# Performance work log

Hardware: AMD Instinct MI355X
Metric: run time of the kernel (lower is better)

The kernel has to match this reference:

```python
import jax, jax.numpy as jnp
import numpy as np

PS = 16          # patch size == conv kernel == stride
EPS = 1e-5       # BatchNorm eps (torch default)


def setup_inputs() -> dict:
    key = jax.random.key(0)
    ks = jax.random.split(key, 12)
    B, Cin, H = 64, 3, 256
    D, Dm = 3, 768                      # private_depth, hidden_dim
    P = (H // PS) ** 2                  # num_patches = 256

    x = jax.random.normal(ks[0], (B, Cin, H, H), jnp.float32)
    # patch-embed conv: weight [O, I, kh, kw], bias [O]
    conv0_w = jax.random.normal(ks[1], (Dm, Cin, PS, PS), jnp.float32) * 0.02
    conv0_b = jax.random.normal(ks[2], (Dm,), jnp.float32) * 0.02
    # depth x (1x1 conv + BN): stacked params
    w1 = jax.random.normal(ks[3], (D, Dm, Dm), jnp.float32) * 0.02   # [O, I]
    b1 = jax.random.normal(ks[4], (D, Dm), jnp.float32) * 0.02
    gamma = jnp.ones((D, Dm), jnp.float32)
    beta = jnp.zeros((D, Dm), jnp.float32)
    # positional embedding [1, P, Dm]
    pos_emb = jax.random.normal(ks[5], (1, P, Dm), jnp.float32)
    # mixer Linear [out, in] + bias
    mixer_w = jax.random.normal(ks[6], (Dm, Dm), jnp.float32) * 0.02
    mixer_b = jax.random.normal(ks[7], (Dm,), jnp.float32) * 0.02
    # per-sample random permutation of the P patches (replaces randperm loop)
    perm = jax.vmap(lambda k: jax.random.permutation(k, P))(
        jax.random.split(ks[8], B)).astype(jnp.int32)

    return {"x": x, "conv0_w": conv0_w, "conv0_b": conv0_b, "w1": w1,
            "b1": b1, "gamma": gamma, "beta": beta, "pos_emb": pos_emb,
            "mixer_w": mixer_w, "mixer_b": mixer_b, "perm": perm}


def reference(x, conv0_w, conv0_b, w1, b1, gamma, beta, pos_emb,
              mixer_w, mixer_b, perm):
    B, Cin, H, W = x.shape
    hp, wp = H // PS, W // PS
    Dm = conv0_w.shape[0]

    # non-overlapping patch conv == reshape + matmul
    # x -> [B, hp*wp, Cin*PS*PS] with (c, kh, kw) flattening matching conv weight
    patches = x.reshape(B, Cin, hp, PS, wp, PS).transpose(0, 2, 4, 1, 3, 5)
    patches = patches.reshape(B, hp * wp, Cin * PS * PS)
    h = jax.nn.relu(patches @ conv0_w.reshape(Dm, -1).T + conv0_b)  # [B, P, Dm]

    # private_depth x (1x1 conv -> BN (batch stats, no running stats) -> ReLU)
    for d in range(w1.shape[0]):
        h = h @ w1[d].T + b1[d]
        mu = h.mean(axis=(0, 1))                      # per-channel over (B, H*W)
        var = ((h - mu) ** 2).mean(axis=(0, 1))       # biased variance
        h = (h - mu) * jax.lax.rsqrt(var + EPS) * gamma[d] + beta[d]
        h = jax.nn.relu(h)

    # pos embedding + mixer (ReLU -> Linear)
    h = h + pos_emb
    h = jax.nn.relu(h) @ mixer_w.T + mixer_b          # [B, P, Dm]

    # per-sample pixel shuffle: shuffled[i, j] = h[i, perm[i, j]]
    out = jnp.take_along_axis(h, perm[:, :, None].astype(jnp.int32), axis=1)
    return out
```

## Files before the change

### kernel.cpp

```cpp
#include <hip/hip_runtime.h>
#include <hip/hip_bf16.h>
#include <stdint.h>

#define M_TOT 16384
#define DM 768
#define BM 128
#define BN 192
#define NKT3 12
#define QOFF (128 * DM)

typedef __attribute__((ext_vector_type(4))) float f32x4;
typedef __attribute__((ext_vector_type(8))) short short8;
typedef __attribute__((ext_vector_type(8))) unsigned short ushort8;
typedef __attribute__((ext_vector_type(4))) unsigned short ushort4v;

__device__ __forceinline__ unsigned short f2bf(float f) {
    union { float f; unsigned u; } v; v.f = f;
    unsigned r = v.u + 0x7fffu + ((v.u >> 16) & 1u);
    return (unsigned short)(r >> 16);
}
__device__ __forceinline__ float bf2f(unsigned short h) {
    union { unsigned u; float f; } v; v.u = ((unsigned)h) << 16;
    return v.f;
}

__device__ __forceinline__ void gload_lds16(const unsigned short* g, unsigned short* l) {
    __builtin_amdgcn_global_load_lds(
        (const __attribute__((address_space(1))) void*)g,
        (__attribute__((address_space(3))) void*)l, 16, 0, 0);
}

__global__ __launch_bounds__(256)
void prepw(const float* __restrict__ cw, const float* __restrict__ w1,
           const float* __restrict__ mw, const int* __restrict__ perm,
           unsigned short* __restrict__ wA, unsigned short* __restrict__ wD,
           unsigned short* __restrict__ wM, int* __restrict__ invp)
{
    int b = blockIdx.x;
    if (b < 2880) {
        int i = b * 256 + threadIdx.x;
        const float* src; unsigned short* dst; int off;
        if (i < 147456)              { src = cw; dst = wA; off = i; }
        else if (i < 147456+442368)  { src = w1; dst = wD; off = i - 147456; }
        else                         { src = mw; dst = wM; off = i - 589824; }
        f32x4 v = ((const f32x4*)src)[off];
        ushort4v o;
        o.x = f2bf(v.x); o.y = f2bf(v.y); o.z = f2bf(v.z); o.w = f2bf(v.w);
        ((ushort4v*)dst)[off] = o;
    } else {
        int i = (b - 2880) * 256 + threadIdx.x;
        int bb = i >> 8;
        invp[(bb << 8) + perm[i]] = i & 255;
    }
}

#define VM0  asm volatile("s_waitcnt vmcnt(0)" ::: "memory");
#define LGKM0 asm volatile("s_waitcnt lgkmcnt(0)" ::: "memory");
#define BARR asm volatile("s_barrier" ::: "memory");

#define PH(AB, BB, MH, KS, LOADB, PRE, POST)                                     \
  {                                                                              \
    if (LOADB) {                                                                 \
      _Pragma("unroll")                                                          \
      for (int j = 0; j < 3; ++j)                                                \
        breg[j] = *(const short8*)((const char*)Bb + (size_t)(BB) * (BN*64*2) +  \
                  (wc * 48 + j * 16 + frow) * 128 + (((KS) * 64 + fq16) ^ rswz));\
    }                                                                            \
    short8 af[4];                                                                \
    _Pragma("unroll")                                                            \
    for (int i = 0; i < 4; ++i)                                                  \
      af[i] = *(const short8*)((const char*)Aa + (size_t)(AB) * (BM*64*2) +      \
              ((MH) * 64 + i * 16 + frow) * 128 +                                \
              (((KS) * 64 + fq16) ^ rswz));                                      \
    PRE;                                                                         \
    __builtin_amdgcn_s_setprio(1);                                               \
    _Pragma("unroll")                                                            \
    for (int i = 0; i < 4; ++i)                                                  \
      _Pragma("unroll")                                                          \
      for (int j = 0; j < 3; ++j)                                                \
        acc[(MH) * 4 + i][j] = __builtin_amdgcn_mfma_f32_16x16x32_bf16(          \
            af[i], breg[j], acc[(MH) * 4 + i][j], 0, 0, 0);                      \
    __builtin_amdgcn_s_setprio(0);                                               \
    POST;                                                                        \
    BARR                                                                         \
  }

#define ALOADM(t, S)                                                             \
  {                                                                              \
    if (XF == 3) {                                                               \
      const int c  = (t) >> 2;                                                   \
      const int r  = ((t) & 3) * 64 + (lane & 7) * 8;                            \
      const int kh = r >> 4;                                                     \
      const int kw0 = r & 15;                                                    \
      _Pragma("unroll")                                                          \
      for (int j = 0; j < 4; ++j) {                                              \
        int m = m0 + rRow0 + j * 8;                                              \
        int b = m >> 8, p = m & 255;                                             \
        const float* src = X + ((((size_t)b * 3 + c) * 256 + (p >> 4) * 16 + kh) \
                                * 256 + (p & 15) * 16 + kw0);                    \
        aldf##S[j][0] = *(const f32x4*)src;                                      \
        aldf##S[j][1] = *(const f32x4*)(src + 4);                                \
      }                                                                          \
    } else {                                                                     \
      _Pragma("unroll")                                                          \
      for (int j = 0; j < 4; ++j)                                                \
        aldr##S[j] = *(const ushort8*)(gAr + (size_t)j * 8 * DM + (t) * 64);     \
    }                                                                            \
  }

#define XFORMM(t, tb, S)                                                         \
  {                                                                              \
    if (XF == 3) {                                                               \
      _Pragma("unroll")                                                          \
      for (int j = 0; j < 4; ++j) {                                              \
        int row = rRow0 + j * 8;                                                 \
        ushort8 o;                                                               \
        _Pragma("unroll")                                                        \
        for (int e = 0; e < 8; ++e)                                              \
          o[e] = f2bf((e < 4) ? aldf##S[j][0][e] : aldf##S[j][1][e - 4]);        \
        *(ushort8*)((char*)Aa + (size_t)(tb) * (BM*64*2) + row * 128 +           \
                    (((lane & 7) * 16) ^ wrswz)) = o;                            \
      }                                                                          \
    } else {                                                                     \
      const int k0 = (t) * 64 + (lane & 7) * 8;                                  \
      f32x4 sa = *(const f32x4*)(ssA + k0);                                      \
      f32x4 sb = *(const f32x4*)(ssA + k0 + 4);                                  \
      f32x4 ha = *(const f32x4*)(ssA + DM + k0);                                 \
      f32x4 hb = *(const f32x4*)(ssA + DM + k0 + 4);                             \
      _Pragma("unroll")                                                          \
      for (int j = 0; j < 4; ++j) {                                              \
        int row = rRow0 + j * 8;                                                 \
        ushort8 u = aldr##S[j];                                                  \
        ushort8 o;                                                               \
        _Pragma("unroll")                                                        \
        for (int e = 0; e < 8; ++e) {                                            \
          float f = bf2f(u[e]);                                                  \
          float sc = (e < 4) ? sa[e] : sb[e - 4];                                \
          float sh = (e < 4) ? ha[e] : hb[e - 4];                                \
          o[e] = f2bf(fmaxf(fmaf(sc, f, sh), 0.0f));                             \
        }                                                                        \
        *(ushort8*)((char*)Aa + (size_t)(tb) * (BM*64*2) + row * 128 +           \
                    (((lane & 7) * 16) ^ wrswz)) = o;                            \
      }                                                                          \
    }                                                                            \
  }

#define XTILE(kt, CB, LS, XS)                                                    \
    PH(CB, CB, 0, 0, 1, { if ((kt) < 11) STAGE_B((CB) ^ 1, (kt) + 1);            \
                          if ((kt) < 10) ALOADM((kt) + 2, LS) }, {})             \
    PH(CB, CB, 1, 0, 0, { if ((kt) < 11) XFORMM((kt) + 1, (CB) ^ 1, XS) },       \
                        { if ((kt) < 11) LGKM0 })                                \
    PH(CB, CB, 0, 1, 1, {}, {})                                                  \
    if ((kt) < 11) { PH(CB, CB, 1, 1, 0, {}, { VM0 }) }                          \
    else           { PH(CB, CB, 1, 1, 0, {}, {}) }

template<int EPI, int XF>
__global__ __launch_bounds__(256, 2)
void gemm8p(const void* __restrict__ Asrc,
            const unsigned short* __restrict__ Bw,
            const float* __restrict__ bias,
            void* __restrict__ outp,
            const int* __restrict__ invp,
            float* __restrict__ bnpart,
            const float* __restrict__ ssA)
{
    __shared__ unsigned short Aa[2][BM * 64];
    __shared__ unsigned short Bb[2][BN * 64];

    const unsigned short* A = (const unsigned short*)Asrc;
    const float* X = (const float*)Asrc;

    const int tid  = threadIdx.x;
    const int w    = tid >> 6;
    const int lane = tid & 63;
    const int wc = w;

    int bid = blockIdx.x;
    int nb  = (bid & 7) * 64 + (bid >> 3);
    const int tileM = nb >> 2, tileN = nb & 3;
    const int m0 = tileM * BM, n0 = tileN * BN;

    const int sRow = lane >> 3;
    const int swzc = ((lane & 7) * 16) ^ ((sRow & 7) << 4);
    const unsigned short* gA0 = A  + (size_t)(m0 + w * 32 + sRow) * DM + (swzc >> 1);
    const unsigned short* gB0 = Bw + (size_t)(n0 + w * 48 + sRow) * DM + (swzc >> 1);

    auto STAGE_A = [&](int buf, int kt) {
        #pragma unroll
        for (int j = 0; j < 4; ++j)
            gload_lds16(gA0 + (size_t)j * 8 * DM + kt * 64,
                        &Aa[buf][(w * 32 + j * 8) * 64]);
    };
    auto STAGE_B = [&](int buf, int kt) {
        #pragma unroll
        for (int j = 0; j < 6; ++j)
            gload_lds16(gB0 + (size_t)j * 8 * DM + kt * 64,
                        &Bb[buf][(w * 48 + j * 8) * 64]);
    };

    const int rRow0 = w * 32 + (lane >> 3);
    const unsigned short* gAr = A + (size_t)(m0 + rRow0) * DM + (lane & 7) * 8;
    const int wrswz = (lane >> 3) << 4;
    ushort8 aldr0[4], aldr1[4];
    f32x4   aldf0[4][2], aldf1[4][2];

    const int frow = lane & 15;
    const int fq16 = (lane >> 4) * 16;
    const int rswz = (lane & 7) << 4;

    f32x4 acc[8][3] = {};
    short8 breg[3];

    if (XF == 0) {
        STAGE_A(0, 0);
        STAGE_B(0, 0);
        VM0
        BARR
    } else {
        ALOADM(0, 0)
        ALOADM(1, 1)
        STAGE_B(0, 0);
        XFORMM(0, 0, 0)
        VM0
        LGKM0
        BARR
    }

    if (XF == 0) {
        #pragma unroll
        for (int kt = 0; kt < NKT3; ++kt) {
            const int cb = kt & 1, nbuf = cb ^ 1;
            PH(cb, cb, 0, 0, 1, { if (kt < 11) STAGE_B(nbuf, kt + 1); }, {})
            PH(cb, cb, 1, 0, 0, { if (kt < 11) STAGE_A(nbuf, kt + 1); }, {})
            PH(cb, cb, 0, 1, 1, {}, {})
            if (kt < 11) { PH(cb, cb, 1, 1, 0, {}, { VM0 }) }
            else         { PH(cb, cb, 1, 1, 0, {}, {}) }
        }
    } else {
        for (int kp = 0; kp < 6; ++kp) {
            const int kte = 2 * kp;
            XTILE(kte, 0, 0, 1)
            const int kto = kte + 1;
            XTILE(kto, 1, 1, 0)
        }
    }

    const int crow = (lane >> 4) * 4;
    const int ccol = lane & 15;
    const int nbase = n0 + wc * 48;

    float bv[3];
    #pragma unroll
    for (int j = 0; j < 3; ++j) bv[j] = bias[nbase + j * 16 + ccol];

    if (EPI == 0) {
        unsigned short* O = (unsigned short*)outp;
        #pragma unroll
        for (int mi = 0; mi < 8; ++mi) {
            #pragma unroll
            for (int r = 0; r < 4; ++r) {
                int m = m0 + mi * 16 + crow + r;
                unsigned short* orow = O + (size_t)m * DM + nbase + ccol;
                #pragma unroll
                for (int j = 0; j < 3; ++j)
                    orow[j * 16] = f2bf(fmaxf(acc[mi][j][r] + bv[j], 0.0f));
            }
        }
    }

    if (EPI == 2) {
        float* O = (float*)outp;
        #pragma unroll
        for (int mi = 0; mi < 8; ++mi) {
            #pragma unroll
            for (int r = 0; r < 4; ++r) {
                int m = m0 + mi * 16 + crow + r;
                int mo = (m & ~255) | invp[m];
                float* orow = O + (size_t)mo * DM + nbase + ccol;
                #pragma unroll
                for (int j = 0; j < 3; ++j)
                    orow[j * 16] = acc[mi][j][r] + bv[j];
            }
        }
    }

    if (EPI == 1) {
        unsigned short* O = (unsigned short*)outp;
        #pragma unroll
        for (int mi = 0; mi < 8; ++mi) {
            #pragma unroll
            for (int r = 0; r < 4; ++r) {
                int m = m0 + mi * 16 + crow + r;
                unsigned short* orow = O + (size_t)m * DM + nbase + ccol;
                #pragma unroll
                for (int j = 0; j < 3; ++j)
                    orow[j * 16] = f2bf(acc[mi][j][r] + bv[j]);
            }
        }
        #pragma unroll
        for (int j = 0; j < 3; ++j) {
            float s = 0.f, q = 0.f;
            #pragma unroll
            for (int mi = 0; mi < 8; ++mi)
                #pragma unroll
                for (int r = 0; r < 4; ++r) {
                    float v = acc[mi][j][r] + bv[j];
                    s += v; q += v * v;
                }
            s += __shfl_xor(s, 16); s += __shfl_xor(s, 32);
            q += __shfl_xor(q, 16); q += __shfl_xor(q, 32);
            if (lane < 16) {
                int c = nbase + j * 16 + lane;
                bnpart[(size_t)c * 128 + tileM]        = s;
                bnpart[QOFF + (size_t)c * 128 + tileM] = q;
            }
        }
    }
}

__global__ void bn_stats(const float* __restrict__ part, const float* __restrict__ gamma,
                         const float* __restrict__ beta, float* __restrict__ ss)
{
    int c = blockIdx.x * 256 + threadIdx.x;
    const float* ps = part + (size_t)c * 128;
    const float* pq = part + QOFF + (size_t)c * 128;
    float s = 0.f, q = 0.f;
    #pragma unroll 8
    for (int i = 0; i < 128; ++i) { s += ps[i]; q += pq[i]; }
    float mu  = s * (1.0f / 16384.0f);
    float var = q * (1.0f / 16384.0f) - mu * mu;
    float scale = rsqrtf(var + 1e-5f) * gamma[c];
    ss[c] = scale;
    ss[DM + c] = beta[c] - mu * scale;
}

__global__ __launch_bounds__(256)
void bnpos_apply(const unsigned short* __restrict__ hin, const float* __restrict__ ss,
                 const float* __restrict__ pos, unsigned short* __restrict__ hout)
{
    __shared__ float sc[DM], sh[DM];
    const int t = threadIdx.x;
    #pragma unroll
    for (int i = 0; i < 3; ++i) {
        sc[t + i * 256] = ss[t + i * 256];
        sh[t + i * 256] = ss[DM + t + i * 256];
    }
    __syncthreads();

    int g = blockIdx.x * 256 + t;
    int row = g / 96;
    int c0 = (g - row * 96) * 8;
    const short8 v = *(const short8*)(hin + (size_t)row * DM + c0);
    short8 o;
    #pragma unroll
    for (int e = 0; e < 8; ++e) {
        float xv = bf2f((unsigned short)v[e]);
        float y = fmaxf(xv * sc[c0 + e] + sh[c0 + e], 0.0f);
        y = fmaxf(y + pos[(row & 255) * DM + c0 + e], 0.0f);
        o[e] = (short)f2bf(y);
    }
    *(short8*)(hout + (size_t)row * DM + c0) = o;
}

extern "C" void kernel_launch(void* const* d_in, const int* in_sizes, int n_in,
                              void* d_out, int out_size, void* d_ws, size_t ws_size,
                              hipStream_t stream)
{
    (void)in_sizes; (void)n_in; (void)out_size; (void)ws_size;

    const float* x       = (const float*)d_in[0];
    const float* conv0_w = (const float*)d_in[1];
    const float* conv0_b = (const float*)d_in[2];
    const float* w1      = (const float*)d_in[3];
    const float* b1      = (const float*)d_in[4];
    const float* gamma   = (const float*)d_in[5];
    const float* beta    = (const float*)d_in[6];
    const float* pos     = (const float*)d_in[7];
    const float* mixer_w = (const float*)d_in[8];
    const float* mixer_b = (const float*)d_in[9];
    const int*   perm    = (const int*)d_in[10];

    unsigned short* actA = (unsigned short*)d_ws;
    unsigned short* actB = actA + (size_t)M_TOT * DM;
    unsigned short* wA   = actB + (size_t)M_TOT * DM;
    unsigned short* wD   = wA + DM * DM;
    unsigned short* wM   = wD + 3 * DM * DM;
    float* bnpart = (float*)(wM + DM * DM);
    float* ss     = bnpart + 2 * 128 * DM;
    int*   invp   = (int*)(ss + 2 * DM);

    prepw<<<2944, 256, 0, stream>>>(conv0_w, w1, mixer_w, perm, wA, wD, wM, invp);

    gemm8p<0, 3><<<512, 256, 0, stream>>>(x, wA, conv0_b, actB, nullptr,
                                          nullptr, nullptr);
    gemm8p<1, 0><<<512, 256, 0, stream>>>(actB, wD + 0 * (size_t)DM * DM, b1 + 0 * DM,
                                          actA, nullptr, bnpart, nullptr);
    bn_stats<<<3, 256, 0, stream>>>(bnpart, gamma + 0 * DM, beta + 0 * DM, ss);
    gemm8p<1, 1><<<512, 256, 0, stream>>>(actA, wD + 1 * (size_t)DM * DM, b1 + 1 * DM,
                                          actB, nullptr, bnpart, ss);
    bn_stats<<<3, 256, 0, stream>>>(bnpart, gamma + 1 * DM, beta + 1 * DM, ss);
    gemm8p<1, 1><<<512, 256, 0, stream>>>(actB, wD + 2 * (size_t)DM * DM, b1 + 2 * DM,
                                          actA, nullptr, bnpart, ss);
    bn_stats<<<3, 256, 0, stream>>>(bnpart, gamma + 2 * DM, beta + 2 * DM, ss);
    bnpos_apply<<<6144, 256, 0, stream>>>(actA, ss, pos, actB);
    gemm8p<2, 0><<<512, 256, 0, stream>>>(actB, wM, mixer_b, d_out, invp,
                                          nullptr, nullptr);
}
```

Baseline: 185.8 us.

## Restructure GEMM k-loop into two k-halves with one barrier per tile

Replaces the four-phase per-k-tile schedule (each phase loading a 64-row A half plus B fragments and ending in a barrier) with two larger half-K steps. Each step loads all 8 A fragments and 3 B fragments before issuing 24 MFMAs, and the whole tile is synchronised by a single barrier. Global staging of the next tile is issued together at the start of the first half. The aim is fewer barriers and larger MFMA batches, at the cost of more live registers, which may lower occupancy or cause spills, and less interleaving of loads with compute.

```diff
diff --git a/kernel.cpp b/kernel.cpp
--- a/kernel.cpp
+++ b/kernel.cpp
@@ -85,6 +85,28 @@
     BARR                                                                         \
   }
 
+#define KHALF(CB, KS)                                                            \
+  {                                                                              \
+    short8 a8[8], b3[3];                                                         \
+    _Pragma("unroll")                                                            \
+    for (int i = 0; i < 8; ++i)                                                  \
+      a8[i] = *(const short8*)((const char*)Aa + (size_t)(CB) * (BM*64*2) +      \
+              (i * 16 + frow) * 128 + (((KS) * 64 + fq16) ^ rswz));              \
+    _Pragma("unroll")                                                            \
+    for (int j = 0; j < 3; ++j)                                                  \
+      b3[j] = *(const short8*)((const char*)Bb + (size_t)(CB) * (BN*64*2) +      \
+              (wc * 48 + j * 16 + frow) * 128 + (((KS) * 64 + fq16) ^ rswz));    \
+    if (KS == 0 && ktv < 11) { STAGE_B(CB ^ 1, ktv + 1); STAGE_A(CB ^ 1, ktv + 1); } \
+    __builtin_amdgcn_s_setprio(1);                                               \
+    _Pragma("unroll")                                                            \
+    for (int i = 0; i < 8; ++i)                                                  \
+      _Pragma("unroll")                                                          \
+      for (int j = 0; j < 3; ++j)                                                \
+        acc[i][j] = __builtin_amdgcn_mfma_f32_16x16x32_bf16(                     \
+            a8[i], b3[j], acc[i][j], 0, 0, 0);                                   \
+    __builtin_amdgcn_s_setprio(0);                                               \
+  }
+
 #define ALOADM(t, S)                                                             \
   {                                                                              \
     if (XF == 3) {                                                               \
@@ -228,13 +250,12 @@
 
     if (XF == 0) {
         #pragma unroll
-        for (int kt = 0; kt < NKT3; ++kt) {
-            const int cb = kt & 1, nbuf = cb ^ 1;
-            PH(cb, cb, 0, 0, 1, { if (kt < 11) STAGE_B(nbuf, kt + 1); }, {})
-            PH(cb, cb, 1, 0, 0, { if (kt < 11) STAGE_A(nbuf, kt + 1); }, {})
-            PH(cb, cb, 0, 1, 1, {}, {})
-            if (kt < 11) { PH(cb, cb, 1, 1, 0, {}, { VM0 }) }
-            else         { PH(cb, cb, 1, 1, 0, {}, {}) }
+        for (int ktv = 0; ktv < NKT3; ++ktv) {
+            const int cb = ktv & 1;
+            KHALF(cb, 0)
+            KHALF(cb, 1)
+            if (ktv < 11) { VM0 }
+            BARR
         }
     } else {
         for (int kp = 0; kp < 6; ++kp) {
```

Result: no change. 186.0 us, median of 3 (+0.2%).

## Switch GEMM warp tiling to 2x2 layout and cut per-k-tile barriers

Applied to the files above, without the earlier changes.

Each of the four waves previously owned all 128 rows and a 48-column slice. It now owns a 64x96 quadrant, so every wave loads 4 A fragments and 6 B fragments per k-step instead of re-reading A for every column slice. This reduces LDS read traffic per MFMA. The four barrier-separated phases per k-tile collapse into two phases with a single barrier, and the BN partial-stat buffer doubles to hold per-wave-row partials. Costs are higher register pressure from six live B fragments, less fine-grained interleaving of staging with compute, and a longer reduction in bn_stats.

```diff
diff --git a/kernel.cpp b/kernel.cpp
--- a/kernel.cpp
+++ b/kernel.cpp
@@ -7,7 +7,7 @@
 #define BM 128
 #define BN 192
 #define NKT3 12
-#define QOFF (128 * DM)
+#define QOFF (256 * DM)
 
 typedef __attribute__((ext_vector_type(4))) float f32x4;
 typedef __attribute__((ext_vector_type(8))) short short8;
@@ -58,31 +58,27 @@
 #define LGKM0 asm volatile("s_waitcnt lgkmcnt(0)" ::: "memory");
 #define BARR asm volatile("s_barrier" ::: "memory");
 
-#define PH(AB, BB, MH, KS, LOADB, PRE, POST)                                     \
+#define PHASE(CB, KS, PRE, POST)                                                 \
   {                                                                              \
-    if (LOADB) {                                                                 \
-      _Pragma("unroll")                                                          \
-      for (int j = 0; j < 3; ++j)                                                \
-        breg[j] = *(const short8*)((const char*)Bb + (size_t)(BB) * (BN*64*2) +  \
-                  (wc * 48 + j * 16 + frow) * 128 + (((KS) * 64 + fq16) ^ rswz));\
-    }                                                                            \
-    short8 af[4];                                                                \
+    short8 a4[4], b6[6];                                                         \
     _Pragma("unroll")                                                            \
     for (int i = 0; i < 4; ++i)                                                  \
-      af[i] = *(const short8*)((const char*)Aa + (size_t)(AB) * (BM*64*2) +      \
-              ((MH) * 64 + i * 16 + frow) * 128 +                                \
-              (((KS) * 64 + fq16) ^ rswz));                                      \
+      a4[i] = *(const short8*)((const char*)Aa + (size_t)(CB) * (BM*64*2) +      \
+              (wr * 64 + i * 16 + frow) * 128 + (((KS) * 64 + fq16) ^ rswz));    \
+    _Pragma("unroll")                                                            \
+    for (int j = 0; j < 6; ++j)                                                  \
+      b6[j] = *(const short8*)((const char*)Bb + (size_t)(CB) * (BN*64*2) +      \
+              (wc * 96 + j * 16 + frow) * 128 + (((KS) * 64 + fq16) ^ rswz));    \
     PRE;                                                                         \
     __builtin_amdgcn_s_setprio(1);                                               \
     _Pragma("unroll")                                                            \
     for (int i = 0; i < 4; ++i)                                                  \
       _Pragma("unroll")                                                          \
-      for (int j = 0; j < 3; ++j)                                                \
-        acc[(MH) * 4 + i][j] = __builtin_amdgcn_mfma_f32_16x16x32_bf16(          \
-            af[i], breg[j], acc[(MH) * 4 + i][j], 0, 0, 0);                      \
+      for (int j = 0; j < 6; ++j)                                                \
+        acc[i][j] = __builtin_amdgcn_mfma_f32_16x16x32_bf16(                     \
+            a4[i], b6[j], acc[i][j], 0, 0, 0);                                   \
     __builtin_amdgcn_s_setprio(0);                                               \
     POST;                                                                        \
-    BARR                                                                         \
   }
 
 #define ALOADM(t, S)                                                             \
@@ -146,13 +142,11 @@
   }
 
 #define XTILE(kt, CB, LS, XS)                                                    \
-    PH(CB, CB, 0, 0, 1, { if ((kt) < 11) STAGE_B((CB) ^ 1, (kt) + 1);            \
-                          if ((kt) < 10) ALOADM((kt) + 2, LS) }, {})             \
-    PH(CB, CB, 1, 0, 0, { if ((kt) < 11) XFORMM((kt) + 1, (CB) ^ 1, XS) },       \
-                        { if ((kt) < 11) LGKM0 })                                \
-    PH(CB, CB, 0, 1, 1, {}, {})                                                  \
-    if ((kt) < 11) { PH(CB, CB, 1, 1, 0, {}, { VM0 }) }                          \
-    else           { PH(CB, CB, 1, 1, 0, {}, {}) }
+    PHASE(CB, 0, { if ((kt) < 11) STAGE_B((CB) ^ 1, (kt) + 1);                   \
+                   if ((kt) < 10) ALOADM((kt) + 2, LS) }, {})                    \
+    PHASE(CB, 1, { if ((kt) < 11) XFORMM((kt) + 1, (CB) ^ 1, XS) },              \
+                 { if ((kt) < 11) { LGKM0 VM0 } })                               \
+    BARR
 
 template<int EPI, int XF>
 __global__ __launch_bounds__(256, 2)
@@ -173,7 +167,7 @@
     const int tid  = threadIdx.x;
     const int w    = tid >> 6;
     const int lane = tid & 63;
-    const int wc = w;
+    const int wr = w >> 1, wc = w & 1;
 
     int bid = blockIdx.x;
     int nb  = (bid & 7) * 64 + (bid >> 3);
@@ -208,8 +202,7 @@
     const int fq16 = (lane >> 4) * 16;
     const int rswz = (lane & 7) << 4;
 
-    f32x4 acc[8][3] = {};
-    short8 breg[3];
+    f32x4 acc[4][6] = {};
 
     if (XF == 0) {
         STAGE_A(0, 0);
@@ -230,11 +223,9 @@
         #pragma unroll
         for (int kt = 0; kt < NKT3; ++kt) {
             const int cb = kt & 1, nbuf = cb ^ 1;
-            PH(cb, cb, 0, 0, 1, { if (kt < 11) STAGE_B(nbuf, kt + 1); }, {})
-            PH(cb, cb, 1, 0, 0, { if (kt < 11) STAGE_A(nbuf, kt + 1); }, {})
-            PH(cb, cb, 0, 1, 1, {}, {})
-            if (kt < 11) { PH(cb, cb, 1, 1, 0, {}, { VM0 }) }
-            else         { PH(cb, cb, 1, 1, 0, {}, {}) }
+            PHASE(cb, 0, { if (kt < 11) { STAGE_B(nbuf, kt + 1); STAGE_A(nbuf, kt + 1); } }, {})
+            PHASE(cb, 1, {}, { if (kt < 11) VM0 })
+            BARR
         }
     } else {
         for (int kp = 0; kp < 6; ++kp) {
@@ -247,22 +238,22 @@
 
     const int crow = (lane >> 4) * 4;
     const int ccol = lane & 15;
-    const int nbase = n0 + wc * 48;
-
-    float bv[3];
+    const int nbase = n0 + wc * 96;
+
+    float bv[6];
     #pragma unroll
-    for (int j = 0; j < 3; ++j) bv[j] = bias[nbase + j * 16 + ccol];
+    for (int j = 0; j < 6; ++j) bv[j] = bias[nbase + j * 16 + ccol];
 
     if (EPI == 0) {
         unsigned short* O = (unsigned short*)outp;
         #pragma unroll
-        for (int mi = 0; mi < 8; ++mi) {
+        for (int mi = 0; mi < 4; ++mi) {
             #pragma unroll
             for (int r = 0; r < 4; ++r) {
-                int m = m0 + mi * 16 + crow + r;
+                int m = m0 + wr * 64 + mi * 16 + crow + r;
                 unsigned short* orow = O + (size_t)m * DM + nbase + ccol;
                 #pragma unroll
-                for (int j = 0; j < 3; ++j)
+                for (int j = 0; j < 6; ++j)
                     orow[j * 16] = f2bf(fmaxf(acc[mi][j][r] + bv[j], 0.0f));
             }
         }
@@ -271,14 +262,14 @@
     if (EPI == 2) {
         float* O = (float*)outp;
         #pragma unroll
-        for (int mi = 0; mi < 8; ++mi) {
+        for (int mi = 0; mi < 4; ++mi) {
             #pragma unroll
             for (int r = 0; r < 4; ++r) {
-                int m = m0 + mi * 16 + crow + r;
+                int m = m0 + wr * 64 + mi * 16 + crow + r;
                 int mo = (m & ~255) | invp[m];
                 float* orow = O + (size_t)mo * DM + nbase + ccol;
                 #pragma unroll
-                for (int j = 0; j < 3; ++j)
+                for (int j = 0; j < 6; ++j)
                     orow[j * 16] = acc[mi][j][r] + bv[j];
             }
         }
@@ -287,21 +278,21 @@
     if (EPI == 1) {
         unsigned short* O = (unsigned short*)outp;
         #pragma unroll
-        for (int mi = 0; mi < 8; ++mi) {
+        for (int mi = 0; mi < 4; ++mi) {
             #pragma unroll
             for (int r = 0; r < 4; ++r) {
-                int m = m0 + mi * 16 + crow + r;
+                int m = m0 + wr * 64 + mi * 16 + crow + r;
                 unsigned short* orow = O + (size_t)m * DM + nbase + ccol;
                 #pragma unroll
-                for (int j = 0; j < 3; ++j)
+                for (int j = 0; j < 6; ++j)
                     orow[j * 16] = f2bf(acc[mi][j][r] + bv[j]);
             }
         }
         #pragma unroll
-        for (int j = 0; j < 3; ++j) {
+        for (int j = 0; j < 6; ++j) {
             float s = 0.f, q = 0.f;
             #pragma unroll
-            for (int mi = 0; mi < 8; ++mi)
+            for (int mi = 0; mi < 4; ++mi)
                 #pragma unroll
                 for (int r = 0; r < 4; ++r) {
                     float v = acc[mi][j][r] + bv[j];
@@ -310,9 +301,10 @@
             s += __shfl_xor(s, 16); s += __shfl_xor(s, 32);
             q += __shfl_xor(q, 16); q += __shfl_xor(q, 32);
             if (lane < 16) {
-                int c = nbase + j * 16 + lane;
-                bnpart[(size_t)c * 128 + tileM]        = s;
-                bnpart[QOFF + (size_t)c * 128 + tileM] = q;
+                int c  = nbase + j * 16 + lane;
+                int ri = tileM * 2 + wr;
+                bnpart[(size_t)c * 256 + ri]        = s;
+                bnpart[QOFF + (size_t)c * 256 + ri] = q;
             }
         }
     }
@@ -322,11 +314,11 @@
                          const float* __restrict__ beta, float* __restrict__ ss)
 {
     int c = blockIdx.x * 256 + threadIdx.x;
-    const float* ps = part + (size_t)c * 128;
-    const float* pq = part + QOFF + (size_t)c * 128;
+    const float* ps = part + (size_t)c * 256;
+    const float* pq = part + QOFF + (size_t)c * 256;
     float s = 0.f, q = 0.f;
     #pragma unroll 8
-    for (int i = 0; i < 128; ++i) { s += ps[i]; q += pq[i]; }
+    for (int i = 0; i < 256; ++i) { s += ps[i]; q += pq[i]; }
     float mu  = s * (1.0f / 16384.0f);
     float var = q * (1.0f / 16384.0f) - mu * mu;
     float scale = rsqrtf(var + 1e-5f) * gamma[c];
@@ -386,7 +378,7 @@
     unsigned short* wD   = wA + DM * DM;
     unsigned short* wM   = wD + 3 * DM * DM;
     float* bnpart = (float*)(wM + DM * DM);
-    float* ss     = bnpart + 2 * 128 * DM;
+    float* ss     = bnpart + 2 * 256 * DM;
     int*   invp   = (int*)(ss + 2 * DM);
 
     prepw<<<2944, 256, 0, stream>>>(conv0_w, w1, mixer_w, perm, wA, wD, wM, invp);
```

After: 210.3 us. +13.2%, slower.
